# Optimization experiments

Hardware: AMD Instinct MI355X
Metric: run time of the kernel (lower is better)

The kernel has to match this reference:

```python
import jax, jax.numpy as jnp
import numpy as np

B, R, N = 1, 1024, 128
C_FEAT, C_MSA, C_PAIR = 22, 256, 128
NBINS = 65  # relpos bins, vbins = arange(65) - 32


def setup_inputs() -> dict:
    key = jax.random.key(0)
    ks = jax.random.split(key, 9)
    w = lambda k, shape: (jax.random.normal(k, shape, jnp.float32) * 0.05)
    return {
        "target_feat": jax.random.normal(ks[0], (B, R, C_FEAT), jnp.float32),
        "residue_index": jnp.broadcast_to(jnp.arange(R, dtype=jnp.int32), (B, R)),
        "msa_feat": jax.random.normal(ks[1], (B, N, R, C_FEAT), jnp.float32),
        "Wa": w(ks[2], (C_PAIR, C_FEAT)), "ba": jnp.zeros((C_PAIR,), jnp.float32),
        "Wb": w(ks[3], (C_PAIR, C_FEAT)), "bb": jnp.zeros((C_PAIR,), jnp.float32),
        "Wm1": w(ks[4], (C_MSA, C_FEAT)), "bm1": jnp.zeros((C_MSA,), jnp.float32),
        "Wm2": w(ks[5], (C_MSA, C_FEAT)), "bm2": jnp.zeros((C_MSA,), jnp.float32),
        "Wpos": w(ks[6], (C_PAIR, NBINS)), "bpos": jnp.zeros((C_PAIR,), jnp.float32),
    }


def reference(target_feat, residue_index, msa_feat,
              Wa, ba, Wb, bb, Wm1, bm1, Wm2, bm2, Wpos, bpos):
    # pair init: z[b,i,j] = to_a(tf)[b,j] + to_b(tf)[b,i]
    a = target_feat @ Wa.T + ba                      # (b, r, c_pair)
    bv = target_feat @ Wb.T + bb                     # (b, r, c_pair)
    z = a[:, None, :, :] + bv[:, :, None, :]         # (b, r, r, c_pair)

    # relpos: nearest-bin one-hot of d = ri[j] - ri[i] against arange(65)-32,
    # then Linear(65 -> c_pair).  One-hot @ W.T is exactly an embedding gather
    # of row clip(d+32, 0, 64) from Wpos.T, so skip materializing the one-hot.
    d = residue_index[:, None, :] - residue_index[:, :, None]  # (b, r, r)
    bins = jnp.clip(d + (NBINS // 2), 0, NBINS - 1)            # (b, r, r) int
    z = z + Wpos.T[bins] + bpos                                # gather + bias

    # MSA init: m = to_m1(msa_feat) + to_m2(target_feat) broadcast over n rows
    m = (msa_feat @ Wm1.T + bm1) + (target_feat @ Wm2.T + bm2)[:, None, :, :]
    return m, z
```

## Files before the change

### kernel.cpp

```cpp
#include <hip/hip_runtime.h>

#define RR     1024
#define NSEQ   128
#define CFEAT  22
#define CMSA   256
#define CPAIR  128
#define NBINS  65

typedef float f4 __attribute__((ext_vector_type(4)));

__global__ __launch_bounds__(256) void k_pre(
    const float* __restrict__ tf,
    const float* __restrict__ Wa, const float* __restrict__ ba,
    const float* __restrict__ Wb, const float* __restrict__ bb,
    const float* __restrict__ Wm2, const float* __restrict__ bm2,
    const float* __restrict__ Wpos, const float* __restrict__ bpos,
    float* __restrict__ a, float* __restrict__ bvp,
    float* __restrict__ tm2, float* __restrict__ pose)
{
    __shared__ float wlds[CFEAT][512];
    __shared__ float rows[8][CFEAT];
    const int t = threadIdx.x;
    const int r0 = blockIdx.x * 8;

    for (int idx = t; idx < 128 * CFEAT; idx += 256) {
        int c = idx / CFEAT, k = idx - c * CFEAT;
        wlds[k][c] = Wa[idx];
    }
    for (int idx = t; idx < 128 * CFEAT; idx += 256) {
        int c = idx / CFEAT, k = idx - c * CFEAT;
        wlds[k][128 + c] = Wb[idx];
    }
    for (int idx = t; idx < 256 * CFEAT; idx += 256) {
        int c = idx / CFEAT, k = idx - c * CFEAT;
        wlds[k][256 + c] = Wm2[idx];
    }
    for (int idx = t; idx < 8 * CFEAT; idx += 256) {
        int rr = idx / CFEAT, k = idx - rr * CFEAT;
        rows[rr][k] = tf[(r0 + rr) * CFEAT + k];
    }
    __syncthreads();

    #pragma unroll
    for (int rr = 0; rr < 8; ++rr) {
        const int r = r0 + rr;
        float s1 = 0.f, s2 = 0.f;
        #pragma unroll
        for (int k = 0; k < CFEAT; ++k) {
            float rv = rows[rr][k];
            s1 += rv * wlds[k][t];
            s2 += rv * wlds[k][256 + t];
        }
        tm2[r * CMSA + t] = s2 + bm2[t];
        if (t < CPAIR) a[r * CPAIR + t] = s1 + ba[t];
        else           bvp[r * CPAIR + (t - CPAIR)] = s1 + bb[t - CPAIR];
    }

    if (blockIdx.x < NBINS && t < CPAIR)
        pose[blockIdx.x * CPAIR + t] = Wpos[t * NBINS + blockIdx.x] + bpos[t];
}

#define PPB 64
__global__ __launch_bounds__(256) void k_msa(
    const float* __restrict__ msa,
    const float* __restrict__ Wm1, const float* __restrict__ bm1,
    const float* __restrict__ tm2, float* __restrict__ out_m)
{
    __shared__ float wt[CFEAT][CMSA];
    __shared__ float rows[PPB][24];
    const int t = threadIdx.x;

    for (int idx = t; idx < CMSA * CFEAT; idx += 256) {
        int c = idx / CFEAT, k = idx - c * CFEAT;
        wt[k][c] = Wm1[idx];
    }
    const long pbase = (long)blockIdx.x * PPB;
    const float* src = msa + pbase * CFEAT;
    for (int idx = t; idx < PPB * CFEAT; idx += 256) {
        int p = idx / CFEAT, k = idx - p * CFEAT;
        rows[p][k] = src[idx];
    }
    if (t < PPB) { rows[t][22] = 0.f; rows[t][23] = 0.f; }
    __syncthreads();

    const int c  = (t & 63) * 4;
    const int wv = t >> 6;

    f4 wr[24];
    #pragma unroll
    for (int k = 0; k < CFEAT; ++k) wr[k] = *(const f4*)&wt[k][c];
    wr[22] = (f4){0.f, 0.f, 0.f, 0.f};
    wr[23] = (f4){0.f, 0.f, 0.f, 0.f};
    const f4 b4 = *(const f4*)(bm1 + c);

    for (int it = 0; it < PPB / 4; ++it) {
        const int p = it * 4 + wv;
        const long pair = pbase + p;
        const int r = (int)(pair & (RR - 1));
        f4 acc = (f4){0.f, 0.f, 0.f, 0.f};
        #pragma unroll
        for (int k4 = 0; k4 < 6; ++k4) {
            f4 mv = *(const f4*)&rows[p][k4 * 4];
            acc += mv.x * wr[k4 * 4 + 0];
            acc += mv.y * wr[k4 * 4 + 1];
            acc += mv.z * wr[k4 * 4 + 2];
            acc += mv.w * wr[k4 * 4 + 3];
        }
        const f4 t4 = *(const f4*)(tm2 + (long)r * CMSA + c);
        f4 o = acc + b4 + t4;
        __builtin_nontemporal_store(o, (f4*)(out_m + pair * CMSA + c));
    }
}

__global__ __launch_bounds__(512) void k_pair(
    const int* __restrict__ resi,
    const float* __restrict__ a, const float* __restrict__ bvp,
    const float* __restrict__ pose, float* __restrict__ out_z)
{
    __shared__ float poseL[NBINS][CPAIR];
    __shared__ int   rjL[RR];
    const int i = blockIdx.x;
    const int t = threadIdx.x;

    for (int idx = t; idx < NBINS * CPAIR; idx += 512)
        (&poseL[0][0])[idx] = pose[idx];
    for (int idx = t; idx < RR; idx += 512)
        rjL[idx] = resi[idx];
    __syncthreads();

    const int c4 = (t & 31) * 4;
    const int jo = t >> 5;
    const int ri = rjL[i];
    const f4 bvv = *(const f4*)(bvp + (long)i * CPAIR + c4);
    float* dst = out_z + (long)i * RR * CPAIR;

    #pragma unroll 4
    for (int jj = 0; jj < RR; jj += 16) {
        const int j = jj + jo;
        int d = rjL[j] - ri + (NBINS / 2);
        d = min(max(d, 0), NBINS - 1);
        const f4 av = *(const f4*)(a + (long)j * CPAIR + c4);
        const f4 pv = *(const f4*)&poseL[d][c4];
        f4 o = av + bvv + pv;
        __builtin_nontemporal_store(o, (f4*)(dst + (long)j * CPAIR + c4));
    }
}

extern "C" void kernel_launch(void* const* d_in, const int* in_sizes, int n_in,
                              void* d_out, int out_size, void* d_ws, size_t ws_size,
                              hipStream_t stream) {
    const float* tf   = (const float*)d_in[0];
    const int*   resi = (const int*)  d_in[1];
    const float* msa  = (const float*)d_in[2];
    const float* Wa   = (const float*)d_in[3];
    const float* ba   = (const float*)d_in[4];
    const float* Wb   = (const float*)d_in[5];
    const float* bb   = (const float*)d_in[6];
    const float* Wm1  = (const float*)d_in[7];
    const float* bm1  = (const float*)d_in[8];
    const float* Wm2  = (const float*)d_in[9];
    const float* bm2  = (const float*)d_in[10];
    const float* Wpos = (const float*)d_in[11];
    const float* bpos = (const float*)d_in[12];

    float* out_m = (float*)d_out;
    float* out_z = out_m + (long)NSEQ * RR * CMSA;

    float* a    = (float*)d_ws;
    float* bvp  = a   + (long)RR * CPAIR;
    float* tm2  = bvp + (long)RR * CPAIR;
    float* pose = tm2 + (long)RR * CMSA;

    k_pre<<<128, 256, 0, stream>>>(tf, Wa, ba, Wb, bb, Wm2, bm2, Wpos, bpos,
                                   a, bvp, tm2, pose);
    k_msa<<<(NSEQ * RR) / PPB, 256, 0, stream>>>(msa, Wm1, bm1, tm2, out_m);
    k_pair<<<RR, 512, 0, stream>>>(resi, a, bvp, pose, out_z);
}
```

Baseline: 157.2 us.

## Fuse MSA and pair kernels into one interleaved launch

Merges the MSA projection and pair-writing kernels into a single 4096-block launch, alternating groups of 8 blocks between the two roles so both write streams run concurrently. Pair blocks now cover half a row (512 j) with 256 threads and read the pose table from global/L2 instead of staging it in LDS. The goal is to remove the serialization and tail between the two store-bound kernels. LDS is shared via a union sized for the MSA role, and the pose gathers become global loads.

```diff
diff --git a/kernel.cpp b/kernel.cpp
--- a/kernel.cpp
+++ b/kernel.cpp
@@ -61,88 +61,88 @@
 }
 
 #define PPB 64
-__global__ __launch_bounds__(256) void k_msa(
+
+__global__ __launch_bounds__(256) void k_fused(
+    const int* __restrict__ resi,
+    const float* __restrict__ a, const float* __restrict__ bvp,
+    const float* __restrict__ pose, float* __restrict__ out_z,
     const float* __restrict__ msa,
     const float* __restrict__ Wm1, const float* __restrict__ bm1,
     const float* __restrict__ tm2, float* __restrict__ out_m)
 {
-    __shared__ float wt[CFEAT][CMSA];
-    __shared__ float rows[PPB][24];
+    __shared__ union U {
+        struct { float wt[CFEAT][CMSA]; float rows[PPB][24]; } m;
+        struct { int rj[512]; } p;
+    } sm;
+    const int bx = blockIdx.x;
+    const int grp = bx >> 3, sub = bx & 7;
+    const int id = (grp >> 1) * 8 + sub;
     const int t = threadIdx.x;
 
-    for (int idx = t; idx < CMSA * CFEAT; idx += 256) {
-        int c = idx / CFEAT, k = idx - c * CFEAT;
-        wt[k][c] = Wm1[idx];
-    }
-    const long pbase = (long)blockIdx.x * PPB;
-    const float* src = msa + pbase * CFEAT;
-    for (int idx = t; idx < PPB * CFEAT; idx += 256) {
-        int p = idx / CFEAT, k = idx - p * CFEAT;
-        rows[p][k] = src[idx];
-    }
-    if (t < PPB) { rows[t][22] = 0.f; rows[t][23] = 0.f; }
-    __syncthreads();
+    if ((grp & 1) == 0) {
+        const int i = id >> 1;
+        const int jbase = (id & 1) * 512;
+        for (int idx = t; idx < 512; idx += 256)
+            sm.p.rj[idx] = resi[jbase + idx];
+        __syncthreads();
 
-    const int c  = (t & 63) * 4;
-    const int wv = t >> 6;
+        const int c4 = (t & 31) * 4;
+        const int jo = t >> 5;
+        const int ri = resi[i];
+        const f4 bvv = *(const f4*)(bvp + (long)i * CPAIR + c4);
+        float* dst = out_z + ((long)i * RR + jbase) * CPAIR;
 
-    f4 wr[24];
-    #pragma unroll
-    for (int k = 0; k < CFEAT; ++k) wr[k] = *(const f4*)&wt[k][c];
-    wr[22] = (f4){0.f, 0.f, 0.f, 0.f};
-    wr[23] = (f4){0.f, 0.f, 0.f, 0.f};
-    const f4 b4 = *(const f4*)(bm1 + c);
+        #pragma unroll 4
+        for (int jj = 0; jj < 512; jj += 8) {
+            const int jl = jj + jo;
+            int d = sm.p.rj[jl] - ri + (NBINS / 2);
+            d = min(max(d, 0), NBINS - 1);
+            const f4 av = *(const f4*)(a + (long)(jbase + jl) * CPAIR + c4);
+            const f4 pv = *(const f4*)(pose + (long)d * CPAIR + c4);
+            f4 o = av + bvv + pv;
+            __builtin_nontemporal_store(o, (f4*)(dst + (long)jl * CPAIR + c4));
+        }
+    } else {
+        for (int idx = t; idx < CMSA * CFEAT; idx += 256) {
+            int c = idx / CFEAT, k = idx - c * CFEAT;
+            sm.m.wt[k][c] = Wm1[idx];
+        }
+        const long pbase = (long)id * PPB;
+        const float* src = msa + pbase * CFEAT;
+        for (int idx = t; idx < PPB * CFEAT; idx += 256) {
+            int p = idx / CFEAT, k = idx - p * CFEAT;
+            sm.m.rows[p][k] = src[idx];
+        }
+        if (t < PPB) { sm.m.rows[t][22] = 0.f; sm.m.rows[t][23] = 0.f; }
+        __syncthreads();
 
-    for (int it = 0; it < PPB / 4; ++it) {
-        const int p = it * 4 + wv;
-        const long pair = pbase + p;
-        const int r = (int)(pair & (RR - 1));
-        f4 acc = (f4){0.f, 0.f, 0.f, 0.f};
+        const int c  = (t & 63) * 4;
+        const int wv = t >> 6;
+
+        f4 wr[24];
         #pragma unroll
-        for (int k4 = 0; k4 < 6; ++k4) {
-            f4 mv = *(const f4*)&rows[p][k4 * 4];
-            acc += mv.x * wr[k4 * 4 + 0];
-            acc += mv.y * wr[k4 * 4 + 1];
-            acc += mv.z * wr[k4 * 4 + 2];
-            acc += mv.w * wr[k4 * 4 + 3];
+        for (int k = 0; k < CFEAT; ++k) wr[k] = *(const f4*)&sm.m.wt[k][c];
+        wr[22] = (f4){0.f, 0.f, 0.f, 0.f};
+        wr[23] = (f4){0.f, 0.f, 0.f, 0.f};
+        const f4 b4 = *(const f4*)(bm1 + c);
+
+        for (int it = 0; it < PPB / 4; ++it) {
+            const int p = it * 4 + wv;
+            const long pair = pbase + p;
+            const int r = (int)(pair & (RR - 1));
+            f4 acc = (f4){0.f, 0.f, 0.f, 0.f};
+            #pragma unroll
+            for (int k4 = 0; k4 < 6; ++k4) {
+                f4 mv = *(const f4*)&sm.m.rows[p][k4 * 4];
+                acc += mv.x * wr[k4 * 4 + 0];
+                acc += mv.y * wr[k4 * 4 + 1];
+                acc += mv.z * wr[k4 * 4 + 2];
+                acc += mv.w * wr[k4 * 4 + 3];
+            }
+            const f4 t4 = *(const f4*)(tm2 + (long)r * CMSA + c);
+            f4 o = acc + b4 + t4;
+            __builtin_nontemporal_store(o, (f4*)(out_m + pair * CMSA + c));
         }
-        const f4 t4 = *(const f4*)(tm2 + (long)r * CMSA + c);
-        f4 o = acc + b4 + t4;
-        __builtin_nontemporal_store(o, (f4*)(out_m + pair * CMSA + c));
-    }
-}
-
-__global__ __launch_bounds__(512) void k_pair(
-    const int* __restrict__ resi,
-    const float* __restrict__ a, const float* __restrict__ bvp,
-    const float* __restrict__ pose, float* __restrict__ out_z)
-{
-    __shared__ float poseL[NBINS][CPAIR];
-    __shared__ int   rjL[RR];
-    const int i = blockIdx.x;
-    const int t = threadIdx.x;
-
-    for (int idx = t; idx < NBINS * CPAIR; idx += 512)
-        (&poseL[0][0])[idx] = pose[idx];
-    for (int idx = t; idx < RR; idx += 512)
-        rjL[idx] = resi[idx];
-    __syncthreads();
-
-    const int c4 = (t & 31) * 4;
-    const int jo = t >> 5;
-    const int ri = rjL[i];
-    const f4 bvv = *(const f4*)(bvp + (long)i * CPAIR + c4);
-    float* dst = out_z + (long)i * RR * CPAIR;
-
-    #pragma unroll 4
-    for (int jj = 0; jj < RR; jj += 16) {
-        const int j = jj + jo;
-        int d = rjL[j] - ri + (NBINS / 2);
-        d = min(max(d, 0), NBINS - 1);
-        const f4 av = *(const f4*)(a + (long)j * CPAIR + c4);
-        const f4 pv = *(const f4*)&poseL[d][c4];
-        f4 o = av + bvv + pv;
-        __builtin_nontemporal_store(o, (f4*)(dst + (long)j * CPAIR + c4));
     }
 }
 
@@ -173,6 +173,6 @@
 
     k_pre<<<128, 256, 0, stream>>>(tf, Wa, ba, Wb, bb, Wm2, bm2, Wpos, bpos,
                                    a, bvp, tm2, pose);
-    k_msa<<<(NSEQ * RR) / PPB, 256, 0, stream>>>(msa, Wm1, bm1, tm2, out_m);
-    k_pair<<<RR, 512, 0, stream>>>(resi, a, bvp, pose, out_z);
+    k_fused<<<4096, 256, 0, stream>>>(resi, a, bvp, pose, out_z,
+                                      msa, Wm1, bm1, tm2, out_m);
 }
```

Measured after the change: 147.7 us. 6.0% less time.
